# Kernel optimization log

Hardware: AMD Instinct MI355X
Metric: run time of the kernel (lower is better)

Reference implementation:

```python
import jax, jax.numpy as jnp
import numpy as np


def setup_inputs() -> dict:
    key = jax.random.key(0)
    kq, kk, kv = jax.random.split(key, 3)
    B, H, S, D = 4, 16, 2048, 64
    q = jax.random.normal(kq, (B, H, S, D), dtype=jnp.float32)
    k = jax.random.normal(kk, (B, H, S, D), dtype=jnp.float32)
    v = jax.random.normal(kv, (B, H, S, D), dtype=jnp.float32)
    return {"q": q, "k": k, "v": v}


def reference(q, k, v):
    # SplitScaleAttend (inference, no mask, no dropout):
    # softmax(q k^T / sqrt(d)) v — the chunked loop in the original is a
    # memory-saving schedule of the same math, so one fused expression here.
    scale = q.shape[-1] ** (-0.5)
    # (b h i d),(b h j d) -> (b h i j)
    sim = jnp.einsum("bhid,bhjd->bhij", q, k * scale)
    attn = jax.nn.softmax(sim, axis=-1)
    # (b h i j),(b h j d) -> (b h i d)
    return jnp.einsum("bhij,bhjd->bhid", attn, v)
```

## Files before the change

kernel.cpp:

```cpp
#include <hip/hip_runtime.h>
#include <hip/hip_bf16.h>

typedef __attribute__((ext_vector_type(8))) short short8_t;
typedef __attribute__((ext_vector_type(4))) float f32x4;
typedef __attribute__((ext_vector_type(16))) float f32x16;
typedef __attribute__((ext_vector_type(4))) unsigned u32x4;

static constexpr int B = 4, H = 16, S = 2048, D = 64;
static constexpr int WAVES = 4, QW = 64, QBLK = WAVES * QW;
static constexpr int KVBLK = 64, NT = S / KVBLK;
static constexpr int LDK = 72;

#define QSCALE 0.18033688011112042f

__device__ __forceinline__ unsigned pk2(float a, float b) {
    __hip_bfloat162 h = __float22bfloat162_rn(float2{a, b});
    unsigned u;
    __builtin_memcpy(&u, &h, 4);
    return u;
}

__device__ __forceinline__ float fexp2(float x) {
#if __has_builtin(__builtin_amdgcn_exp2f)
    return __builtin_amdgcn_exp2f(x);
#else
    return exp2f(x);
#endif
}

__device__ __forceinline__ float frcp(float x) {
#if __has_builtin(__builtin_amdgcn_rcpf)
    return __builtin_amdgcn_rcpf(x);
#else
    return 1.f / x;
#endif
}

#define QK_MFMA(KH, S0, S1)                                                              \
    do {                                                                                 \
        __builtin_amdgcn_s_setprio(1);                                                   \
        _Pragma("unroll")                                                                \
        for (int kc = 0; kc < 4; ++kc) {                                                 \
            const short8_t ka = *reinterpret_cast<const short8_t*>(                      \
                &Ks[cb][(KH) * 32 + ql][kc * 16 + hi * 8]);                              \
            S0 = __builtin_amdgcn_mfma_f32_32x32x16_bf16(ka, qf0[kc], S0, 0, 0, 0);      \
            S1 = __builtin_amdgcn_mfma_f32_32x32x16_bf16(ka, qf1[kc], S1, 0, 0, 0);      \
        }                                                                                \
        __builtin_amdgcn_s_setprio(0);                                                   \
    } while (0)

#define EXP_PACK(S0, S1, CD0, CD1)                                                       \
    do {                                                                                 \
        _Pragma("unroll")                                                                \
        for (int r = 0; r < 16; ++r) S0[r] = fexp2(S0[r]);                               \
        _Pragma("unroll")                                                                \
        for (int r = 0; r < 16; ++r) S1[r] = fexp2(S1[r]);                               \
        _Pragma("unroll")                                                                \
        for (int jj = 0; jj < 8; ++jj) {                                                 \
            CD0[jj] = pk2(S0[jj * 2], S0[jj * 2 + 1]);                                   \
            CD1[jj] = pk2(S1[jj * 2], S1[jj * 2 + 1]);                                   \
        }                                                                                \
    } while (0)

#define PV2(CD0, CD1, KS)                                                                \
    do {                                                                                 \
        const int h_ = (KS) & 1;                                                         \
        const short8_t vfa =                                                             \
            *reinterpret_cast<const short8_t*>(&Vt[cb][ql][(KS) * 16 + hi * 8]);         \
        const short8_t vfb =                                                             \
            *reinterpret_cast<const short8_t*>(&Vt[cb][32 + ql][(KS) * 16 + hi * 8]);    \
        {                                                                                \
            unsigned x0 = CD0[4 * h_ + 0], y0 = CD0[4 * h_ + 2];                         \
            unsigned x1 = CD0[4 * h_ + 1], y1 = CD0[4 * h_ + 3];                         \
            asm volatile("v_permlane32_swap_b32 %0, %1" : "+v"(x0), "+v"(y0));           \
            asm volatile("v_permlane32_swap_b32 %0, %1" : "+v"(x1), "+v"(y1));           \
            const u32x4 pu = {x0, x1, y0, y1};                                           \
            const short8_t pa = __builtin_bit_cast(short8_t, pu);                        \
            Od00 = __builtin_amdgcn_mfma_f32_32x32x16_bf16(pa, vfa, Od00, 0, 0, 0);      \
            Od01 = __builtin_amdgcn_mfma_f32_32x32x16_bf16(pa, vfb, Od01, 0, 0, 0);      \
            Ol0  = __builtin_amdgcn_mfma_f32_32x32x16_bf16(pa, onesf, Ol0, 0, 0, 0);     \
        }                                                                                \
        {                                                                                \
            unsigned x0 = CD1[4 * h_ + 0], y0 = CD1[4 * h_ + 2];                         \
            unsigned x1 = CD1[4 * h_ + 1], y1 = CD1[4 * h_ + 3];                         \
            asm volatile("v_permlane32_swap_b32 %0, %1" : "+v"(x0), "+v"(y0));           \
            asm volatile("v_permlane32_swap_b32 %0, %1" : "+v"(x1), "+v"(y1));           \
            const u32x4 pu = {x0, x1, y0, y1};                                           \
            const short8_t pa = __builtin_bit_cast(short8_t, pu);                        \
            Od10 = __builtin_amdgcn_mfma_f32_32x32x16_bf16(pa, vfa, Od10, 0, 0, 0);      \
            Od11 = __builtin_amdgcn_mfma_f32_32x32x16_bf16(pa, vfb, Od11, 0, 0, 0);      \
            Ol1  = __builtin_amdgcn_mfma_f32_32x32x16_bf16(pa, onesf, Ol1, 0, 0, 0);     \
        }                                                                                \
    } while (0)

__global__ void __launch_bounds__(256, 2)
attn_fwd(const float* __restrict__ q, const float* __restrict__ k,
         const float* __restrict__ v, float* __restrict__ out) {
    __shared__ short Ks[2][KVBLK][LDK];
    __shared__ short Vt[2][D][LDK];

    const int tid  = threadIdx.x;
    const int lane = tid & 63;
    const int ql   = lane & 31;
    const int hi   = lane >> 5;
    const int wave = tid >> 6;

    const int lid = blockIdx.x;
    const int bh  = (lid & 7) | ((lid >> 6) << 3);
    const int qx  = (lid >> 3) & 7;

    const long base = (long)bh * S * D;
    const int  q0w  = qx * QBLK + wave * QW;

    const u32x4 ones_u = {0x3F803F80u, 0x3F803F80u, 0x3F803F80u, 0x3F803F80u};
    const short8_t onesf = __builtin_bit_cast(short8_t, ones_u);

    short8_t qf0[4], qf1[4];
    #pragma unroll
    for (int qb = 0; qb < 2; ++qb) {
        const float* qp = q + base + (long)(q0w + qb * 32 + ql) * D;
        #pragma unroll
        for (int kc = 0; kc < 4; ++kc) {
            const f32x4 a = *reinterpret_cast<const f32x4*>(qp + kc * 16 + hi * 8);
            const f32x4 b = *reinterpret_cast<const f32x4*>(qp + kc * 16 + hi * 8 + 4);
            const u32x4 u = {pk2(a[0] * QSCALE, a[1] * QSCALE),
                             pk2(a[2] * QSCALE, a[3] * QSCALE),
                             pk2(b[0] * QSCALE, b[1] * QSCALE),
                             pk2(b[2] * QSCALE, b[3] * QSCALE)};
            if (qb == 0) qf0[kc] = __builtin_bit_cast(short8_t, u);
            else         qf1[kc] = __builtin_bit_cast(short8_t, u);
        }
    }

    f32x16 Od00, Od01, Ol0, Od10, Od11, Ol1;
    #pragma unroll
    for (int r = 0; r < 16; ++r) {
        Od00[r] = 0.f; Od01[r] = 0.f; Ol0[r] = 0.f;
        Od10[r] = 0.f; Od11[r] = 0.f; Ol1[r] = 0.f;
    }

    const int kr  = tid >> 2,       kc0 = (tid & 3) * 16;
    const int vk2 = (tid & 31) * 2, vd0 = (tid >> 5) * 8;
    const float* kptr  = k + base + (long)kr * D + kc0;
    const float* vptrA = v + base + (long)vk2 * D + vd0;

    f32x4 kfa = *reinterpret_cast<const f32x4*>(kptr);
    f32x4 kfb = *reinterpret_cast<const f32x4*>(kptr + 4);
    f32x4 kfc = *reinterpret_cast<const f32x4*>(kptr + 8);
    f32x4 kfd = *reinterpret_cast<const f32x4*>(kptr + 12);
    f32x4 vfa0 = *reinterpret_cast<const f32x4*>(vptrA);
    f32x4 vfa1 = *reinterpret_cast<const f32x4*>(vptrA + 4);
    f32x4 vfb0 = *reinterpret_cast<const f32x4*>(vptrA + D);
    f32x4 vfb1 = *reinterpret_cast<const f32x4*>(vptrA + D + 4);

    for (int t = 0; t < NT; ++t) {
        const int cb = t & 1;
        {
            const u32x4 ku0 = {pk2(kfa[0], kfa[1]), pk2(kfa[2], kfa[3]),
                               pk2(kfb[0], kfb[1]), pk2(kfb[2], kfb[3])};
            const u32x4 ku1 = {pk2(kfc[0], kfc[1]), pk2(kfc[2], kfc[3]),
                               pk2(kfd[0], kfd[1]), pk2(kfd[2], kfd[3])};
            *reinterpret_cast<u32x4*>(&Ks[cb][kr][kc0])     = ku0;
            *reinterpret_cast<u32x4*>(&Ks[cb][kr][kc0 + 8]) = ku1;
            #pragma unroll
            for (int j = 0; j < 4; ++j) {
                *reinterpret_cast<unsigned*>(&Vt[cb][vd0 + j][vk2])     = pk2(vfa0[j], vfb0[j]);
                *reinterpret_cast<unsigned*>(&Vt[cb][vd0 + 4 + j][vk2]) = pk2(vfa1[j], vfb1[j]);
            }
        }
        __syncthreads();

        if (t + 1 < NT) {
            kptr  += KVBLK * D;
            vptrA += KVBLK * D;
            kfa = *reinterpret_cast<const f32x4*>(kptr);
            kfb = *reinterpret_cast<const f32x4*>(kptr + 4);
            kfc = *reinterpret_cast<const f32x4*>(kptr + 8);
            kfd = *reinterpret_cast<const f32x4*>(kptr + 12);
            vfa0 = *reinterpret_cast<const f32x4*>(vptrA);
            vfa1 = *reinterpret_cast<const f32x4*>(vptrA + 4);
            vfb0 = *reinterpret_cast<const f32x4*>(vptrA + D);
            vfb1 = *reinterpret_cast<const f32x4*>(vptrA + D + 4);
        }

        unsigned cdA0[8], cdA1[8], cdB0[8], cdB1[8];
        {
            f32x16 s0, s1;
            #pragma unroll
            for (int r = 0; r < 16; ++r) { s0[r] = 0.f; s1[r] = 0.f; }
            QK_MFMA(0, s0, s1);
            EXP_PACK(s0, s1, cdA0, cdA1);
        }
        {
            f32x16 s0, s1;
            #pragma unroll
            for (int r = 0; r < 16; ++r) { s0[r] = 0.f; s1[r] = 0.f; }
            QK_MFMA(1, s0, s1);
            EXP_PACK(s0, s1, cdB0, cdB1);
        }

        __builtin_amdgcn_s_setprio(1);
        PV2(cdA0, cdA1, 0);
        PV2(cdA0, cdA1, 1);
        PV2(cdB0, cdB1, 2);
        PV2(cdB0, cdB1, 3);
        __builtin_amdgcn_s_setprio(0);
    }

    {
        float* op = out + base + (long)q0w * D + ql;
        #pragma unroll
        for (int r = 0; r < 16; ++r) {
            const int   row = (r & 3) + 8 * (r >> 2) + 4 * hi;
            const float s   = frcp(Ol0[r]);
            op[(long)row * D]      = Od00[r] * s;
            op[(long)row * D + 32] = Od01[r] * s;
        }
        float* op1 = op + 32 * D;
        #pragma unroll
        for (int r = 0; r < 16; ++r) {
            const int   row = (r & 3) + 8 * (r >> 2) + 4 * hi;
            const float s   = frcp(Ol1[r]);
            op1[(long)row * D]      = Od10[r] * s;
            op1[(long)row * D + 32] = Od11[r] * s;
        }
    }
}

extern "C" void kernel_launch(void* const* d_in, const int* in_sizes, int n_in,
                              void* d_out, int out_size, void* d_ws, size_t ws_size,
                              hipStream_t stream) {
    const float* q = (const float*)d_in[0];
    const float* k = (const float*)d_in[1];
    const float* v = (const float*)d_in[2];
    float* out = (float*)d_out;
    attn_fwd<<<dim3((S / QBLK) * B * H), 256, 0, stream>>>(q, k, v, out);
}
```

Measured before the change: 95.83 us.

## Defer PV MFMAs of previous KV tile into next iteration before barrier

The P·V matrix multiplies for tile t-1 now run at the start of iteration t, after the LDS stores for tile t and before the barrier, reading the other LDS buffer. The last tile's PV is issued after the loop. The aim is to overlap PV MFMA work with the LDS staging and barrier wait, so the matrix unit is not idle around the sync. In exchange, the packed probability registers stay live across the barrier, which raises register pressure under the 2-blocks-per-CU launch bound.

```diff
diff --git a/kernel.cpp b/kernel.cpp
--- a/kernel.cpp
+++ b/kernel.cpp
@@ -36,13 +36,13 @@
 #endif
 }
 
-#define QK_MFMA(KH, S0, S1)                                                              \
+#define QK_MFMA(CB, KH, S0, S1)                                                          \
     do {                                                                                 \
         __builtin_amdgcn_s_setprio(1);                                                   \
         _Pragma("unroll")                                                                \
         for (int kc = 0; kc < 4; ++kc) {                                                 \
             const short8_t ka = *reinterpret_cast<const short8_t*>(                      \
-                &Ks[cb][(KH) * 32 + ql][kc * 16 + hi * 8]);                              \
+                &Ks[CB][(KH) * 32 + ql][kc * 16 + hi * 8]);                              \
             S0 = __builtin_amdgcn_mfma_f32_32x32x16_bf16(ka, qf0[kc], S0, 0, 0, 0);      \
             S1 = __builtin_amdgcn_mfma_f32_32x32x16_bf16(ka, qf1[kc], S1, 0, 0, 0);      \
         }                                                                                \
@@ -62,13 +62,13 @@
         }                                                                                \
     } while (0)
 
-#define PV2(CD0, CD1, KS)                                                                \
+#define PV2(PB, CD0, CD1, KS)                                                            \
     do {                                                                                 \
         const int h_ = (KS) & 1;                                                         \
         const short8_t vfa =                                                             \
-            *reinterpret_cast<const short8_t*>(&Vt[cb][ql][(KS) * 16 + hi * 8]);         \
+            *reinterpret_cast<const short8_t*>(&Vt[PB][ql][(KS) * 16 + hi * 8]);         \
         const short8_t vfb =                                                             \
-            *reinterpret_cast<const short8_t*>(&Vt[cb][32 + ql][(KS) * 16 + hi * 8]);    \
+            *reinterpret_cast<const short8_t*>(&Vt[PB][32 + ql][(KS) * 16 + hi * 8]);    \
         {                                                                                \
             unsigned x0 = CD0[4 * h_ + 0], y0 = CD0[4 * h_ + 2];                         \
             unsigned x1 = CD0[4 * h_ + 1], y1 = CD0[4 * h_ + 3];                         \
@@ -103,14 +103,13 @@
     const int lane = tid & 63;
     const int ql   = lane & 31;
     const int hi   = lane >> 5;
-    const int wave = tid >> 6;
 
     const int lid = blockIdx.x;
     const int bh  = (lid & 7) | ((lid >> 6) << 3);
     const int qx  = (lid >> 3) & 7;
 
     const long base = (long)bh * S * D;
-    const int  q0w  = qx * QBLK + wave * QW;
+    const int  q0w  = qx * QBLK + (tid >> 6) * QW;
 
     const u32x4 ones_u = {0x3F803F80u, 0x3F803F80u, 0x3F803F80u, 0x3F803F80u};
     const short8_t onesf = __builtin_bit_cast(short8_t, ones_u);
@@ -153,6 +152,8 @@
     f32x4 vfb0 = *reinterpret_cast<const f32x4*>(vptrA + D);
     f32x4 vfb1 = *reinterpret_cast<const f32x4*>(vptrA + D + 4);
 
+    unsigned cdA0[8], cdA1[8], cdB0[8], cdB1[8];
+
     for (int t = 0; t < NT; ++t) {
         const int cb = t & 1;
         {
@@ -168,6 +169,16 @@
                 *reinterpret_cast<unsigned*>(&Vt[cb][vd0 + 4 + j][vk2]) = pk2(vfa1[j], vfb1[j]);
             }
         }
+
+        if (t) {
+            __builtin_amdgcn_s_setprio(1);
+            PV2(cb ^ 1, cdA0, cdA1, 0);
+            PV2(cb ^ 1, cdA0, cdA1, 1);
+            PV2(cb ^ 1, cdB0, cdB1, 2);
+            PV2(cb ^ 1, cdB0, cdB1, 3);
+            __builtin_amdgcn_s_setprio(0);
+        }
+
         __syncthreads();
 
         if (t + 1 < NT) {
@@ -183,29 +194,28 @@
             vfb1 = *reinterpret_cast<const f32x4*>(vptrA + D + 4);
         }
 
-        unsigned cdA0[8], cdA1[8], cdB0[8], cdB1[8];
         {
             f32x16 s0, s1;
             #pragma unroll
             for (int r = 0; r < 16; ++r) { s0[r] = 0.f; s1[r] = 0.f; }
-            QK_MFMA(0, s0, s1);
+            QK_MFMA(cb, 0, s0, s1);
             EXP_PACK(s0, s1, cdA0, cdA1);
         }
         {
             f32x16 s0, s1;
             #pragma unroll
             for (int r = 0; r < 16; ++r) { s0[r] = 0.f; s1[r] = 0.f; }
-            QK_MFMA(1, s0, s1);
+            QK_MFMA(cb, 1, s0, s1);
             EXP_PACK(s0, s1, cdB0, cdB1);
         }
-
-        __builtin_amdgcn_s_setprio(1);
-        PV2(cdA0, cdA1, 0);
-        PV2(cdA0, cdA1, 1);
-        PV2(cdB0, cdB1, 2);
-        PV2(cdB0, cdB1, 3);
-        __builtin_amdgcn_s_setprio(0);
-    }
+    }
+
+    __builtin_amdgcn_s_setprio(1);
+    PV2((NT - 1) & 1, cdA0, cdA1, 0);
+    PV2((NT - 1) & 1, cdA0, cdA1, 1);
+    PV2((NT - 1) & 1, cdB0, cdB1, 2);
+    PV2((NT - 1) & 1, cdB0, cdB1, 3);
+    __builtin_amdgcn_s_setprio(0);
 
     {
         float* op = out + base + (long)q0w * D + ql;
```

Result: no change. 95.94 us (+0.1%).

## Double KV tile to 128 rows and interleave QK/PV per 32-key sub-block

Applied to the files above, without the earlier changes.

Raises the KV tile from 64 to 128 keys, halving the number of tile iterations and __syncthreads barriers, and widens the V transpose buffer to match. Global loads are now converted to bf16 immediately into packed registers, so fewer registers sit idle while staging. The QK and PV work is restructured into four sub-blocks, each doing QK then exp then PV, which shortens the live range of P fragments. The cost is doubled LDS usage per block, which may limit occupancy at 2 blocks per CU, plus wider per-thread load and store sequences.

```diff
diff --git a/kernel.cpp b/kernel.cpp
--- a/kernel.cpp
+++ b/kernel.cpp
@@ -8,8 +8,9 @@
 
 static constexpr int B = 4, H = 16, S = 2048, D = 64;
 static constexpr int WAVES = 4, QW = 64, QBLK = WAVES * QW;
-static constexpr int KVBLK = 64, NT = S / KVBLK;
+static constexpr int KVBLK = 128, NT = S / KVBLK;
 static constexpr int LDK = 72;
+static constexpr int LDV = 136;
 
 #define QSCALE 0.18033688011112042f
 
@@ -97,20 +98,19 @@
 attn_fwd(const float* __restrict__ q, const float* __restrict__ k,
          const float* __restrict__ v, float* __restrict__ out) {
     __shared__ short Ks[2][KVBLK][LDK];
-    __shared__ short Vt[2][D][LDK];
+    __shared__ short Vt[2][D][LDV];
 
     const int tid  = threadIdx.x;
     const int lane = tid & 63;
     const int ql   = lane & 31;
     const int hi   = lane >> 5;
-    const int wave = tid >> 6;
 
     const int lid = blockIdx.x;
     const int bh  = (lid & 7) | ((lid >> 6) << 3);
     const int qx  = (lid >> 3) & 7;
 
     const long base = (long)bh * S * D;
-    const int  q0w  = qx * QBLK + wave * QW;
+    const int  q0w  = qx * QBLK + (tid >> 6) * QW;
 
     const u32x4 ones_u = {0x3F803F80u, 0x3F803F80u, 0x3F803F80u, 0x3F803F80u};
     const short8_t onesf = __builtin_bit_cast(short8_t, ones_u);
@@ -139,72 +139,77 @@
         Od10[r] = 0.f; Od11[r] = 0.f; Ol1[r] = 0.f;
     }
 
-    const int kr  = tid >> 2,       kc0 = (tid & 3) * 16;
-    const int vk2 = (tid & 31) * 2, vd0 = (tid >> 5) * 8;
+    const int kr  = tid >> 1,       kc0 = (tid & 1) * 32;
+    const int vk2 = (tid & 63) * 2, vd0 = (tid >> 6) * 16;
     const float* kptr  = k + base + (long)kr * D + kc0;
     const float* vptrA = v + base + (long)vk2 * D + vd0;
 
-    f32x4 kfa = *reinterpret_cast<const f32x4*>(kptr);
-    f32x4 kfb = *reinterpret_cast<const f32x4*>(kptr + 4);
-    f32x4 kfc = *reinterpret_cast<const f32x4*>(kptr + 8);
-    f32x4 kfd = *reinterpret_cast<const f32x4*>(kptr + 12);
-    f32x4 vfa0 = *reinterpret_cast<const f32x4*>(vptrA);
-    f32x4 vfa1 = *reinterpret_cast<const f32x4*>(vptrA + 4);
-    f32x4 vfb0 = *reinterpret_cast<const f32x4*>(vptrA + D);
-    f32x4 vfb1 = *reinterpret_cast<const f32x4*>(vptrA + D + 4);
+    unsigned ks[16], vs[16];
+
+    {
+        #pragma unroll
+        for (int c = 0; c < 4; ++c) {
+            const f32x4 a = *reinterpret_cast<const f32x4*>(kptr + c * 8);
+            const f32x4 b = *reinterpret_cast<const f32x4*>(kptr + c * 8 + 4);
+            ks[c * 4 + 0] = pk2(a[0], a[1]); ks[c * 4 + 1] = pk2(a[2], a[3]);
+            ks[c * 4 + 2] = pk2(b[0], b[1]); ks[c * 4 + 3] = pk2(b[2], b[3]);
+        }
+        #pragma unroll
+        for (int c = 0; c < 4; ++c) {
+            const f32x4 a = *reinterpret_cast<const f32x4*>(vptrA + c * 4);
+            const f32x4 b = *reinterpret_cast<const f32x4*>(vptrA + D + c * 4);
+            #pragma unroll
+            for (int j = 0; j < 4; ++j) vs[c * 4 + j] = pk2(a[j], b[j]);
+        }
+    }
 
     for (int t = 0; t < NT; ++t) {
         const int cb = t & 1;
         {
-            const u32x4 ku0 = {pk2(kfa[0], kfa[1]), pk2(kfa[2], kfa[3]),
-                               pk2(kfb[0], kfb[1]), pk2(kfb[2], kfb[3])};
-            const u32x4 ku1 = {pk2(kfc[0], kfc[1]), pk2(kfc[2], kfc[3]),
-                               pk2(kfd[0], kfd[1]), pk2(kfd[2], kfd[3])};
-            *reinterpret_cast<u32x4*>(&Ks[cb][kr][kc0])     = ku0;
-            *reinterpret_cast<u32x4*>(&Ks[cb][kr][kc0 + 8]) = ku1;
-            #pragma unroll
-            for (int j = 0; j < 4; ++j) {
-                *reinterpret_cast<unsigned*>(&Vt[cb][vd0 + j][vk2])     = pk2(vfa0[j], vfb0[j]);
-                *reinterpret_cast<unsigned*>(&Vt[cb][vd0 + 4 + j][vk2]) = pk2(vfa1[j], vfb1[j]);
-            }
+            #pragma unroll
+            for (int c = 0; c < 4; ++c)
+                *reinterpret_cast<u32x4*>(&Ks[cb][kr][kc0 + c * 8]) =
+                    u32x4{ks[c * 4], ks[c * 4 + 1], ks[c * 4 + 2], ks[c * 4 + 3]};
+            #pragma unroll
+            for (int j = 0; j < 16; ++j)
+                *reinterpret_cast<unsigned*>(&Vt[cb][vd0 + j][vk2]) = vs[j];
         }
         __syncthreads();
 
         if (t + 1 < NT) {
             kptr  += KVBLK * D;
             vptrA += KVBLK * D;
-            kfa = *reinterpret_cast<const f32x4*>(kptr);
-            kfb = *reinterpret_cast<const f32x4*>(kptr + 4);
-            kfc = *reinterpret_cast<const f32x4*>(kptr + 8);
-            kfd = *reinterpret_cast<const f32x4*>(kptr + 12);
-            vfa0 = *reinterpret_cast<const f32x4*>(vptrA);
-            vfa1 = *reinterpret_cast<const f32x4*>(vptrA + 4);
-            vfb0 = *reinterpret_cast<const f32x4*>(vptrA + D);
-            vfb1 = *reinterpret_cast<const f32x4*>(vptrA + D + 4);
-        }
-
-        unsigned cdA0[8], cdA1[8], cdB0[8], cdB1[8];
-        {
+            #pragma unroll
+            for (int c = 0; c < 4; ++c) {
+                const f32x4 a = *reinterpret_cast<const f32x4*>(kptr + c * 8);
+                const f32x4 b = *reinterpret_cast<const f32x4*>(kptr + c * 8 + 4);
+                ks[c * 4 + 0] = pk2(a[0], a[1]); ks[c * 4 + 1] = pk2(a[2], a[3]);
+                ks[c * 4 + 2] = pk2(b[0], b[1]); ks[c * 4 + 3] = pk2(b[2], b[3]);
+            }
+            #pragma unroll
+            for (int c = 0; c < 4; ++c) {
+                const f32x4 a = *reinterpret_cast<const f32x4*>(vptrA + c * 4);
+                const f32x4 b = *reinterpret_cast<const f32x4*>(vptrA + D + c * 4);
+                #pragma unroll
+                for (int j = 0; j < 4; ++j) vs[c * 4 + j] = pk2(a[j], b[j]);
+            }
+        }
+
+        #pragma unroll
+        for (int kh = 0; kh < 4; ++kh) {
             f32x16 s0, s1;
             #pragma unroll
             for (int r = 0; r < 16; ++r) { s0[r] = 0.f; s1[r] = 0.f; }
-            QK_MFMA(0, s0, s1);
-            EXP_PACK(s0, s1, cdA0, cdA1);
-        }
-        {
-            f32x16 s0, s1;
-            #pragma unroll
-            for (int r = 0; r < 16; ++r) { s0[r] = 0.f; s1[r] = 0.f; }
-            QK_MFMA(1, s0, s1);
-            EXP_PACK(s0, s1, cdB0, cdB1);
-        }
-
-        __builtin_amdgcn_s_setprio(1);
-        PV2(cdA0, cdA1, 0);
-        PV2(cdA0, cdA1, 1);
-        PV2(cdB0, cdB1, 2);
-        PV2(cdB0, cdB1, 3);
-        __builtin_amdgcn_s_setprio(0);
+            QK_MFMA(kh, s0, s1);
+
+            unsigned cd0[8], cd1[8];
+            EXP_PACK(s0, s1, cd0, cd1);
+
+            __builtin_amdgcn_s_setprio(1);
+            PV2(cd0, cd1, 2 * kh);
+            PV2(cd0, cd1, 2 * kh + 1);
+            __builtin_amdgcn_s_setprio(0);
+        }
     }
 
     {
```

Measured after the change: 111.6 us. +16.5%, slower.

## Replace ones-MFMA row sums with VALU accumulation and interleave exp with PV

Applied to the files above, without the earlier changes.

The softmax denominator was computed with an extra MFMA against a ones matrix for every PV step. It is now accumulated as fp32 partial sums of the exponentials in each lane. At the end, the two lane halves are combined with a cross-lane shuffle, and the reciprocals are broadcast to all lanes through a small shared-memory table. Both QK halves are now issued before any exponentials, so the exp and pack of the second half can overlap with the PV MFMAs of the first. This removes a third of the PV matrix ops and two accumulator tiles, but adds VALU adds and keeps more score registers live at once.

```diff
diff --git a/kernel.cpp b/kernel.cpp
--- a/kernel.cpp
+++ b/kernel.cpp
@@ -49,12 +49,23 @@
         __builtin_amdgcn_s_setprio(0);                                                   \
     } while (0)
 
-#define EXP_PACK(S0, S1, CD0, CD1)                                                       \
+#define EXP_SUM_PACK(S0, S1, CD0, CD1)                                                   \
     do {                                                                                 \
-        _Pragma("unroll")                                                                \
-        for (int r = 0; r < 16; ++r) S0[r] = fexp2(S0[r]);                               \
-        _Pragma("unroll")                                                                \
-        for (int r = 0; r < 16; ++r) S1[r] = fexp2(S1[r]);                               \
+        float a0 = 0.f, a1 = 0.f, b0 = 0.f, b1 = 0.f;                                    \
+        _Pragma("unroll")                                                                \
+        for (int r = 0; r < 16; ++r) {                                                   \
+            const float e = fexp2(S0[r]);                                                \
+            S0[r] = e;                                                                   \
+            if (r & 1) a1 += e; else a0 += e;                                            \
+        }                                                                                \
+        _Pragma("unroll")                                                                \
+        for (int r = 0; r < 16; ++r) {                                                   \
+            const float e = fexp2(S1[r]);                                                \
+            S1[r] = e;                                                                   \
+            if (r & 1) b1 += e; else b0 += e;                                            \
+        }                                                                                \
+        l0_r += a0 + a1;                                                                 \
+        l1_r += b0 + b1;                                                                 \
         _Pragma("unroll")                                                                \
         for (int jj = 0; jj < 8; ++jj) {                                                 \
             CD0[jj] = pk2(S0[jj * 2], S0[jj * 2 + 1]);                                   \
@@ -78,7 +89,6 @@
             const short8_t pa = __builtin_bit_cast(short8_t, pu);                        \
             Od00 = __builtin_amdgcn_mfma_f32_32x32x16_bf16(pa, vfa, Od00, 0, 0, 0);      \
             Od01 = __builtin_amdgcn_mfma_f32_32x32x16_bf16(pa, vfb, Od01, 0, 0, 0);      \
-            Ol0  = __builtin_amdgcn_mfma_f32_32x32x16_bf16(pa, onesf, Ol0, 0, 0, 0);     \
         }                                                                                \
         {                                                                                \
             unsigned x0 = CD1[4 * h_ + 0], y0 = CD1[4 * h_ + 2];                         \
@@ -89,7 +99,6 @@
             const short8_t pa = __builtin_bit_cast(short8_t, pu);                        \
             Od10 = __builtin_amdgcn_mfma_f32_32x32x16_bf16(pa, vfa, Od10, 0, 0, 0);      \
             Od11 = __builtin_amdgcn_mfma_f32_32x32x16_bf16(pa, vfb, Od11, 0, 0, 0);      \
-            Ol1  = __builtin_amdgcn_mfma_f32_32x32x16_bf16(pa, onesf, Ol1, 0, 0, 0);     \
         }                                                                                \
     } while (0)
 
@@ -98,6 +107,7 @@
          const float* __restrict__ v, float* __restrict__ out) {
     __shared__ short Ks[2][KVBLK][LDK];
     __shared__ short Vt[2][D][LDK];
+    __shared__ float Xl[WAVES][2][32];
 
     const int tid  = threadIdx.x;
     const int lane = tid & 63;
@@ -111,9 +121,6 @@
 
     const long base = (long)bh * S * D;
     const int  q0w  = qx * QBLK + wave * QW;
-
-    const u32x4 ones_u = {0x3F803F80u, 0x3F803F80u, 0x3F803F80u, 0x3F803F80u};
-    const short8_t onesf = __builtin_bit_cast(short8_t, ones_u);
 
     short8_t qf0[4], qf1[4];
     #pragma unroll
@@ -132,12 +139,13 @@
         }
     }
 
-    f32x16 Od00, Od01, Ol0, Od10, Od11, Ol1;
+    f32x16 Od00, Od01, Od10, Od11;
     #pragma unroll
     for (int r = 0; r < 16; ++r) {
-        Od00[r] = 0.f; Od01[r] = 0.f; Ol0[r] = 0.f;
-        Od10[r] = 0.f; Od11[r] = 0.f; Ol1[r] = 0.f;
-    }
+        Od00[r] = 0.f; Od01[r] = 0.f;
+        Od10[r] = 0.f; Od11[r] = 0.f;
+    }
+    float l0_r = 0.f, l1_r = 0.f;
 
     const int kr  = tid >> 2,       kc0 = (tid & 3) * 16;
     const int vk2 = (tid & 31) * 2, vd0 = (tid >> 5) * 8;
@@ -183,36 +191,39 @@
             vfb1 = *reinterpret_cast<const f32x4*>(vptrA + D + 4);
         }
 
-        unsigned cdA0[8], cdA1[8], cdB0[8], cdB1[8];
-        {
-            f32x16 s0, s1;
-            #pragma unroll
-            for (int r = 0; r < 16; ++r) { s0[r] = 0.f; s1[r] = 0.f; }
-            QK_MFMA(0, s0, s1);
-            EXP_PACK(s0, s1, cdA0, cdA1);
-        }
-        {
-            f32x16 s0, s1;
-            #pragma unroll
-            for (int r = 0; r < 16; ++r) { s0[r] = 0.f; s1[r] = 0.f; }
-            QK_MFMA(1, s0, s1);
-            EXP_PACK(s0, s1, cdB0, cdB1);
-        }
-
+        f32x16 sA0, sA1, sB0, sB1;
+        #pragma unroll
+        for (int r = 0; r < 16; ++r) { sA0[r] = 0.f; sA1[r] = 0.f; sB0[r] = 0.f; sB1[r] = 0.f; }
+        QK_MFMA(0, sA0, sA1);
+        QK_MFMA(1, sB0, sB1);
+
+        unsigned cdA0[8], cdA1[8];
+        EXP_SUM_PACK(sA0, sA1, cdA0, cdA1);
         __builtin_amdgcn_s_setprio(1);
         PV2(cdA0, cdA1, 0);
         PV2(cdA0, cdA1, 1);
+        __builtin_amdgcn_s_setprio(0);
+
+        unsigned cdB0[8], cdB1[8];
+        EXP_SUM_PACK(sB0, sB1, cdB0, cdB1);
+        __builtin_amdgcn_s_setprio(1);
         PV2(cdB0, cdB1, 2);
         PV2(cdB0, cdB1, 3);
         __builtin_amdgcn_s_setprio(0);
     }
 
     {
+        const float l0m = l0_r + __shfl_xor(l0_r, 32, 64);
+        const float l1m = l1_r + __shfl_xor(l1_r, 32, 64);
+        if (hi == 0) {
+            Xl[wave][0][ql] = frcp(l0m);
+            Xl[wave][1][ql] = frcp(l1m);
+        }
         float* op = out + base + (long)q0w * D + ql;
         #pragma unroll
         for (int r = 0; r < 16; ++r) {
             const int   row = (r & 3) + 8 * (r >> 2) + 4 * hi;
-            const float s   = frcp(Ol0[r]);
+            const float s   = Xl[wave][0][row];
             op[(long)row * D]      = Od00[r] * s;
             op[(long)row * D + 32] = Od01[r] * s;
         }
@@ -220,7 +231,7 @@
         #pragma unroll
         for (int r = 0; r < 16; ++r) {
             const int   row = (r & 3) + 8 * (r >> 2) + 4 * hi;
-            const float s   = frcp(Ol1[r]);
+            const float s   = Xl[wave][1][row];
             op1[(long)row * D]      = Od10[r] * s;
             op1[(long)row * D + 32] = Od11[r] * s;
         }
```

Result: faster. 91.26 us (-4.8%).
